# Performance work log

Measured on AMD Instinct MI355X. Metric: run time of the kernel, lower is better.

## Reference

```python
import jax, jax.numpy as jnp
import numpy as np

N_NODES = 100000
N_EDGES = 1600000
NEG_SLOPE = 0.2


def gat_conv(x, W, al, ar, src, dst, n_nodes):
    """DGL-style GATConv. x:[N,Fin] W:[Fin,H*D] al,ar:[H,D] -> [N,H,D]."""
    H, D = al.shape
    h = (x @ W).reshape(-1, H, D)                      # [N,H,D]
    el = jnp.sum(h * al, axis=-1)                      # [N,H]
    er = jnp.sum(h * ar, axis=-1)                      # [N,H]
    e = jax.nn.leaky_relu(el[src] + er[dst], NEG_SLOPE)  # [E,H]
    # segment softmax over edges grouped by destination node
    m = jax.ops.segment_max(e, dst, num_segments=n_nodes)  # [N,H]
    ex = jnp.exp(e - m[dst])                           # [E,H]
    s = jax.ops.segment_sum(ex, dst, num_segments=n_nodes)  # [N,H]
    alpha = ex / s[dst]                                # [E,H]
    msg = h[src] * alpha[..., None]                    # [E,H,D]
    return jax.ops.segment_sum(msg, dst, num_segments=n_nodes)  # [N,H,D]


def setup_inputs() -> dict:
    key = jax.random.key(0)
    ks = jax.random.split(key, 9)
    in_dim, hid, out_dim, heads = 128, 32, 64, 4
    x = jax.random.normal(ks[0], (N_NODES, in_dim), dtype=jnp.float32)
    src = jax.random.randint(ks[1], (N_EDGES,), 0, N_NODES, dtype=jnp.int32)
    dst = jax.random.randint(ks[2], (N_EDGES,), 0, N_NODES, dtype=jnp.int32)
    sc1 = 1.0 / np.sqrt(in_dim)
    sc2 = 1.0 / np.sqrt(heads * hid)
    W1 = jax.random.normal(ks[3], (in_dim, heads * hid), dtype=jnp.float32) * sc1
    al1 = jax.random.normal(ks[4], (heads, hid), dtype=jnp.float32) * sc1
    ar1 = jax.random.normal(ks[5], (heads, hid), dtype=jnp.float32) * sc1
    W2 = jax.random.normal(ks[6], (heads * hid, out_dim), dtype=jnp.float32) * sc2
    al2 = jax.random.normal(ks[7], (1, out_dim), dtype=jnp.float32) * sc2
    ar2 = jax.random.normal(ks[8], (1, out_dim), dtype=jnp.float32) * sc2
    return {"x": x, "src": src, "dst": dst, "W1": W1, "al1": al1, "ar1": ar1,
            "W2": W2, "al2": al2, "ar2": ar2}


def reference(x, src, dst, W1, al1, ar1, W2, al2, ar2):
    h = gat_conv(x, W1, al1, ar1, src, dst, N_NODES)   # [N,4,32]
    h = h.reshape(h.shape[0], -1)                      # flatten(1) -> [N,128]
    h = jax.nn.selu(h)                                 # dropout is identity in eval
    out = gat_conv(h, W2, al2, ar2, src, dst, N_NODES) # [N,1,64]
    return out.mean(axis=1)                            # [N,64]
```

## Files before the change

kernel.cpp:

```cpp
#include <hip/hip_runtime.h>
#include <hip/hip_fp16.h>

#define N_NODES 100000
#define N_EDGES 1600000
#define NP1 (N_NODES + 1)
#define SCANB 512
#define NB 391
#define CHUNK 6250
#define NBLK 256

static __device__ __forceinline__ unsigned pkh2(float a, float b) {
    __half2 t = __floats2half2_rn(a, b);
    return *(unsigned*)&t;
}

__global__ __launch_bounds__(256) void k_gemm1(
    const float* __restrict__ x, const float* __restrict__ W,
    const float* __restrict__ al, const float* __restrict__ ar,
    __half* __restrict__ h, float* __restrict__ el, float* __restrict__ er)
{
    __shared__ float xT[32 * 132];
    __shared__ float Wl[32 * 132];
    const int tid = threadIdx.x;
    const int n0 = blockIdx.x * 128;
    const int tc = tid & 15, tr = tid >> 4;
    const int r0 = tr * 8, c0 = tc * 8;

    float acc[8][8];
    #pragma unroll
    for (int i = 0; i < 8; ++i)
        #pragma unroll
        for (int j = 0; j < 8; ++j) acc[i][j] = 0.f;

    for (int kb = 0; kb < 128; kb += 32) {
        {
            const int k4 = (tid & 7) * 4;
            const int rr = tid >> 3;
            #pragma unroll
            for (int ii = 0; ii < 4; ++ii) {
                int row = rr + ii * 32;
                int n = n0 + row;
                float4 v = make_float4(0.f, 0.f, 0.f, 0.f);
                if (n < N_NODES) v = *(const float4*)(x + (size_t)n * 128 + kb + k4);
                xT[(k4 + 0) * 132 + row] = v.x;
                xT[(k4 + 1) * 132 + row] = v.y;
                xT[(k4 + 2) * 132 + row] = v.z;
                xT[(k4 + 3) * 132 + row] = v.w;
            }
        }
        {
            const int c4 = (tid & 31) * 4;
            const int kr = tid >> 5;
            #pragma unroll
            for (int ii = 0; ii < 4; ++ii) {
                int kk = kr + ii * 8;
                float4 w = *(const float4*)(W + (size_t)(kb + kk) * 128 + c4);
                *(float4*)(Wl + kk * 132 + c4) = w;
            }
        }
        __syncthreads();
        #pragma unroll 4
        for (int k = 0; k < 32; ++k) {
            float4 a0 = *(const float4*)(xT + k * 132 + r0);
            float4 a1 = *(const float4*)(xT + k * 132 + r0 + 4);
            float4 b0 = *(const float4*)(Wl + k * 132 + c0);
            float4 b1 = *(const float4*)(Wl + k * 132 + c0 + 4);
            float a[8] = {a0.x, a0.y, a0.z, a0.w, a1.x, a1.y, a1.z, a1.w};
            float b[8] = {b0.x, b0.y, b0.z, b0.w, b1.x, b1.y, b1.z, b1.w};
            #pragma unroll
            for (int i = 0; i < 8; ++i)
                #pragma unroll
                for (int j = 0; j < 8; ++j) acc[i][j] = fmaf(a[i], b[j], acc[i][j]);
        }
        __syncthreads();
    }

    float alv[8], arv[8];
    #pragma unroll
    for (int j = 0; j < 8; ++j) { alv[j] = al[c0 + j]; arv[j] = ar[c0 + j]; }
    #pragma unroll
    for (int i = 0; i < 8; ++i) {
        int n = n0 + r0 + i;
        float pl = 0.f, pr = 0.f;
        #pragma unroll
        for (int j = 0; j < 8; ++j) {
            pl = fmaf(acc[i][j], alv[j], pl);
            pr = fmaf(acc[i][j], arv[j], pr);
        }
        pl += __shfl_xor(pl, 1); pl += __shfl_xor(pl, 2);
        pr += __shfl_xor(pr, 1); pr += __shfl_xor(pr, 2);
        if (n < N_NODES) {
            uint4 o;
            o.x = pkh2(acc[i][0], acc[i][1]);
            o.y = pkh2(acc[i][2], acc[i][3]);
            o.z = pkh2(acc[i][4], acc[i][5]);
            o.w = pkh2(acc[i][6], acc[i][7]);
            *(uint4*)(h + (size_t)n * 128 + c0) = o;
            if ((tc & 3) == 0) {
                el[n * 4 + (tc >> 2)] = pl;
                er[n * 4 + (tc >> 2)] = pr;
            }
        }
    }
}

__global__ __launch_bounds__(256) void k_gemm2(
    const __half* __restrict__ in, const float* __restrict__ W,
    const float* __restrict__ al, const float* __restrict__ ar,
    __half* __restrict__ h, float* __restrict__ el, float* __restrict__ er)
{
    __shared__ float xT[32 * 132];
    __shared__ float Wl[32 * 68];
    const int tid = threadIdx.x;
    const int n0 = blockIdx.x * 128;
    const int tc = tid & 7, tr = tid >> 3;
    const int r0 = tr * 4, c0 = tc * 8;
    const float SC = 1.0507009873554805f;
    const float AL = 1.6732632423543772f;

    float acc[4][8];
    #pragma unroll
    for (int i = 0; i < 4; ++i)
        #pragma unroll
        for (int j = 0; j < 8; ++j) acc[i][j] = 0.f;

    for (int kb = 0; kb < 128; kb += 32) {
        {
            const int k4 = (tid & 7) * 4;
            const int rr = tid >> 3;
            #pragma unroll
            for (int ii = 0; ii < 4; ++ii) {
                int row = rr + ii * 32;
                int n = n0 + row;
                float4 v = make_float4(0.f, 0.f, 0.f, 0.f);
                if (n < N_NODES) {
                    uint2 u = *(const uint2*)(in + (size_t)n * 128 + kb + k4);
                    float2 f01 = __half22float2(*(__half2*)&u.x);
                    float2 f23 = __half22float2(*(__half2*)&u.y);
                    v = make_float4(f01.x, f01.y, f23.x, f23.y);
                }
                v.x = v.x > 0.f ? SC * v.x : SC * AL * (__expf(v.x) - 1.f);
                v.y = v.y > 0.f ? SC * v.y : SC * AL * (__expf(v.y) - 1.f);
                v.z = v.z > 0.f ? SC * v.z : SC * AL * (__expf(v.z) - 1.f);
                v.w = v.w > 0.f ? SC * v.w : SC * AL * (__expf(v.w) - 1.f);
                xT[(k4 + 0) * 132 + row] = v.x;
                xT[(k4 + 1) * 132 + row] = v.y;
                xT[(k4 + 2) * 132 + row] = v.z;
                xT[(k4 + 3) * 132 + row] = v.w;
            }
        }
        {
            const int c4 = (tid & 15) * 4;
            const int kr = tid >> 4;
            #pragma unroll
            for (int ii = 0; ii < 2; ++ii) {
                int kk = kr + ii * 16;
                float4 w = *(const float4*)(W + (size_t)(kb + kk) * 64 + c4);
                *(float4*)(Wl + kk * 68 + c4) = w;
            }
        }
        __syncthreads();
        #pragma unroll 4
        for (int k = 0; k < 32; ++k) {
            float4 a0 = *(const float4*)(xT + k * 132 + r0);
            float4 b0 = *(const float4*)(Wl + k * 68 + c0);
            float4 b1 = *(const float4*)(Wl + k * 68 + c0 + 4);
            float a[4] = {a0.x, a0.y, a0.z, a0.w};
            float b[8] = {b0.x, b0.y, b0.z, b0.w, b1.x, b1.y, b1.z, b1.w};
            #pragma unroll
            for (int i = 0; i < 4; ++i)
                #pragma unroll
                for (int j = 0; j < 8; ++j) acc[i][j] = fmaf(a[i], b[j], acc[i][j]);
        }
        __syncthreads();
    }

    float alv[8], arv[8];
    #pragma unroll
    for (int j = 0; j < 8; ++j) { alv[j] = al[c0 + j]; arv[j] = ar[c0 + j]; }
    #pragma unroll
    for (int i = 0; i < 4; ++i) {
        int n = n0 + r0 + i;
        float pl = 0.f, pr = 0.f;
        #pragma unroll
        for (int j = 0; j < 8; ++j) {
            pl = fmaf(acc[i][j], alv[j], pl);
            pr = fmaf(acc[i][j], arv[j], pr);
        }
        pl += __shfl_xor(pl, 1); pl += __shfl_xor(pl, 2); pl += __shfl_xor(pl, 4);
        pr += __shfl_xor(pr, 1); pr += __shfl_xor(pr, 2); pr += __shfl_xor(pr, 4);
        if (n < N_NODES) {
            uint4 o;
            o.x = pkh2(acc[i][0], acc[i][1]);
            o.y = pkh2(acc[i][2], acc[i][3]);
            o.z = pkh2(acc[i][4], acc[i][5]);
            o.w = pkh2(acc[i][6], acc[i][7]);
            *(uint4*)(h + (size_t)n * 64 + c0) = o;
            if (tc == 0) { el[n] = pl; er[n] = pr; }
        }
    }
}

__global__ __launch_bounds__(SCANB) void k_scan1(
    int* __restrict__ data, int* __restrict__ bsum, int n)
{
    __shared__ int tmp[SCANB];
    int gid = blockIdx.x * SCANB + threadIdx.x;
    int v = (gid < n) ? data[gid] : 0;
    tmp[threadIdx.x] = v;
    __syncthreads();
    for (int off = 1; off < SCANB; off <<= 1) {
        int t = (threadIdx.x >= off) ? tmp[threadIdx.x - off] : 0;
        __syncthreads();
        tmp[threadIdx.x] += t;
        __syncthreads();
    }
    if (gid < n) data[gid] = tmp[threadIdx.x] - v;
    if (threadIdx.x == SCANB - 1) bsum[blockIdx.x] = tmp[SCANB - 1];
}

__global__ __launch_bounds__(256) void k_scan2(int* __restrict__ bsum, int nb)
{
    __shared__ int tmp[256];
    int v = (threadIdx.x < nb) ? bsum[threadIdx.x] : 0;
    tmp[threadIdx.x] = v;
    __syncthreads();
    for (int off = 1; off < 256; off <<= 1) {
        int t = (threadIdx.x >= off) ? tmp[threadIdx.x - off] : 0;
        __syncthreads();
        tmp[threadIdx.x] += t;
        __syncthreads();
    }
    if (threadIdx.x < nb) bsum[threadIdx.x] = tmp[threadIdx.x] - v;
}

__global__ __launch_bounds__(SCANB) void k_scan3(
    int* __restrict__ data, const int* __restrict__ bsum, int n)
{
    int gid = blockIdx.x * SCANB + threadIdx.x;
    if (gid < n) data[gid] += bsum[blockIdx.x];
}

__global__ __launch_bounds__(256) void k_bhist(
    const int* __restrict__ dst, int* __restrict__ bhist)
{
    __shared__ int cnt[NB];
    const int tid = threadIdx.x;
    for (int j = tid; j < NB; j += 256) cnt[j] = 0;
    __syncthreads();
    int beg = blockIdx.x * CHUNK, end = beg + CHUNK;
    for (int i = beg + tid; i < end; i += 256)
        atomicAdd(&cnt[dst[i] >> 8], 1);
    __syncthreads();
    for (int j = tid; j < NB; j += 256)
        bhist[j * NBLK + blockIdx.x] = cnt[j];
}

__global__ __launch_bounds__(256) void k_place(
    const int* __restrict__ src, const int* __restrict__ dst,
    const int* __restrict__ boffs, unsigned* __restrict__ pairs)
{
    __shared__ int cur[NB];
    const int tid = threadIdx.x;
    for (int j = tid; j < NB; j += 256)
        cur[j] = boffs[j * NBLK + blockIdx.x];
    __syncthreads();
    int beg = blockIdx.x * CHUNK, end = beg + CHUNK;
    for (int i = beg + tid; i < end; i += 256) {
        int d = dst[i];
        int p = atomicAdd(&cur[d >> 8], 1);
        pairs[p] = ((unsigned)(d & 255) << 17) | (unsigned)src[i];
    }
}

__global__ __launch_bounds__(256) void k_csr(
    const unsigned* __restrict__ pairs, const int* __restrict__ boffs,
    int* __restrict__ rowptr, int* __restrict__ csr_src)
{
    __shared__ int cnt[256], exc[256];
    const int b = blockIdx.x;
    const int tid = threadIdx.x;
    cnt[tid] = 0;
    __syncthreads();
    int beg = boffs[b * NBLK];
    int end = (b == NB - 1) ? N_EDGES : boffs[(b + 1) * NBLK];
    for (int i = beg + tid; i < end; i += 256)
        atomicAdd(&cnt[pairs[i] >> 17], 1);
    __syncthreads();
    int v = cnt[tid];
    exc[tid] = v;
    __syncthreads();
    for (int o = 1; o < 256; o <<= 1) {
        int t = (tid >= o) ? exc[tid - o] : 0;
        __syncthreads();
        exc[tid] += t;
        __syncthreads();
    }
    int excl = exc[tid] - v;
    int node = b * 256 + tid;
    if (node <= N_NODES) rowptr[node] = beg + excl;
    __syncthreads();
    exc[tid] = beg + excl;
    cnt[tid] = 0;
    __syncthreads();
    for (int i = beg + tid; i < end; i += 256) {
        unsigned e = pairs[i];
        int dl = (int)(e >> 17);
        int r = atomicAdd(&cnt[dl], 1);
        csr_src[exc[dl] + r] = (int)(e & 0x1FFFFu);
    }
}

__global__ __launch_bounds__(256) void k_fused1(
    const int* __restrict__ rowptr, const int* __restrict__ csr_src,
    const __half* __restrict__ h,
    const float* __restrict__ el,
    const float* __restrict__ er,
    __half* __restrict__ out)
{
    __shared__ int   s_sx[4][64];
    __shared__ float s_p[4][64][4];
    const int w = threadIdx.x >> 6;
    int node = (blockIdx.x * 256 + threadIdx.x) >> 6;
    int lane = threadIdx.x & 63;
    if (node >= N_NODES) return;
    int rs = rowptr[node], re = rowptr[node + 1];
    const int q = lane & 15, g = lane >> 4;
    const int hq = q >> 2;
    float4 erd = ((const float4*)er)[node];
    float m0 = -INFINITY, m1 = -INFINITY, m2 = -INFINITY, m3 = -INFINITY;
    float s0 = 0.f, s1 = 0.f, s2 = 0.f, s3 = 0.f;
    float acc[8];
    #pragma unroll
    for (int k = 0; k < 8; ++k) acc[k] = 0.f;

    for (int base = rs; base < re; base += 64) {
        int nch = min(64, re - base);
        int sidx = 0;
        float e0 = -INFINITY, e1 = -INFINITY, e2 = -INFINITY, e3 = -INFINITY;
        if (lane < nch) {
            sidx = csr_src[base + lane];
            float4 l4 = ((const float4*)el)[sidx];
            e0 = l4.x + erd.x; e0 = e0 >= 0.f ? e0 : 0.2f * e0;
            e1 = l4.y + erd.y; e1 = e1 >= 0.f ? e1 : 0.2f * e1;
            e2 = l4.z + erd.z; e2 = e2 >= 0.f ? e2 : 0.2f * e2;
            e3 = l4.w + erd.w; e3 = e3 >= 0.f ? e3 : 0.2f * e3;
        }
        float c0 = e0, c1 = e1, c2 = e2, c3 = e3;
        #pragma unroll
        for (int o = 32; o > 0; o >>= 1) {
            c0 = fmaxf(c0, __shfl_xor(c0, o));
            c1 = fmaxf(c1, __shfl_xor(c1, o));
            c2 = fmaxf(c2, __shfl_xor(c2, o));
            c3 = fmaxf(c3, __shfl_xor(c3, o));
        }
        float n0 = fmaxf(m0, c0), n1 = fmaxf(m1, c1);
        float n2 = fmaxf(m2, c2), n3 = fmaxf(m3, c3);
        float r0 = __expf(m0 - n0), r1 = __expf(m1 - n1);
        float r2 = __expf(m2 - n2), r3 = __expf(m3 - n3);
        float p0 = __expf(e0 - n0), p1 = __expf(e1 - n1);
        float p2 = __expf(e2 - n2), p3 = __expf(e3 - n3);
        s_sx[w][lane] = sidx;
        float4 pv = make_float4(p0, p1, p2, p3);
        *(float4*)&s_p[w][lane][0] = pv;
        float q0 = p0, q1 = p1, q2 = p2, q3 = p3;
        #pragma unroll
        for (int o = 32; o > 0; o >>= 1) {
            q0 += __shfl_xor(q0, o);
            q1 += __shfl_xor(q1, o);
            q2 += __shfl_xor(q2, o);
            q3 += __shfl_xor(q3, o);
        }
        s0 = s0 * r0 + q0; s1 = s1 * r1 + q1;
        s2 = s2 * r2 + q2; s3 = s3 * r3 + q3;
        float rh = hq == 0 ? r0 : hq == 1 ? r1 : hq == 2 ? r2 : r3;
        #pragma unroll
        for (int k = 0; k < 8; ++k) acc[k] *= rh;
        m0 = n0; m1 = n1; m2 = n2; m3 = n3;

        int nit4 = (nch + 15) >> 4;
        for (int t = 0; t < nit4; ++t) {
            int eb = t * 16 + g;
            int sj0 = s_sx[w][eb];
            int sj1 = s_sx[w][eb + 4];
            int sj2 = s_sx[w][eb + 8];
            int sj3 = s_sx[w][eb + 12];
            float a0 = s_p[w][eb][hq];
            float a1 = s_p[w][eb + 4][hq];
            float a2 = s_p[w][eb + 8][hq];
            float a3 = s_p[w][eb + 12][hq];
            uint4 v0 = *((const uint4*)(h + (size_t)sj0 * 128) + q);
            uint4 v1 = *((const uint4*)(h + (size_t)sj1 * 128) + q);
            uint4 v2 = *((const uint4*)(h + (size_t)sj2 * 128) + q);
            uint4 v3 = *((const uint4*)(h + (size_t)sj3 * 128) + q);
            {
                float2 f0 = __half22float2(*(__half2*)&v0.x);
                float2 f1 = __half22float2(*(__half2*)&v0.y);
                float2 f2 = __half22float2(*(__half2*)&v0.z);
                float2 f3 = __half22float2(*(__half2*)&v0.w);
                acc[0] = fmaf(a0, f0.x, acc[0]); acc[1] = fmaf(a0, f0.y, acc[1]);
                acc[2] = fmaf(a0, f1.x, acc[2]); acc[3] = fmaf(a0, f1.y, acc[3]);
                acc[4] = fmaf(a0, f2.x, acc[4]); acc[5] = fmaf(a0, f2.y, acc[5]);
                acc[6] = fmaf(a0, f3.x, acc[6]); acc[7] = fmaf(a0, f3.y, acc[7]);
            }
            {
                float2 f0 = __half22float2(*(__half2*)&v1.x);
                float2 f1 = __half22float2(*(__half2*)&v1.y);
                float2 f2 = __half22float2(*(__half2*)&v1.z);
                float2 f3 = __half22float2(*(__half2*)&v1.w);
                acc[0] = fmaf(a1, f0.x, acc[0]); acc[1] = fmaf(a1, f0.y, acc[1]);
                acc[2] = fmaf(a1, f1.x, acc[2]); acc[3] = fmaf(a1, f1.y, acc[3]);
                acc[4] = fmaf(a1, f2.x, acc[4]); acc[5] = fmaf(a1, f2.y, acc[5]);
                acc[6] = fmaf(a1, f3.x, acc[6]); acc[7] = fmaf(a1, f3.y, acc[7]);
            }
            {
                float2 f0 = __half22float2(*(__half2*)&v2.x);
                float2 f1 = __half22float2(*(__half2*)&v2.y);
                float2 f2 = __half22float2(*(__half2*)&v2.z);
                float2 f3 = __half22float2(*(__half2*)&v2.w);
                acc[0] = fmaf(a2, f0.x, acc[0]); acc[1] = fmaf(a2, f0.y, acc[1]);
                acc[2] = fmaf(a2, f1.x, acc[2]); acc[3] = fmaf(a2, f1.y, acc[3]);
                acc[4] = fmaf(a2, f2.x, acc[4]); acc[5] = fmaf(a2, f2.y, acc[5]);
                acc[6] = fmaf(a2, f3.x, acc[6]); acc[7] = fmaf(a2, f3.y, acc[7]);
            }
            {
                float2 f0 = __half22float2(*(__half2*)&v3.x);
                float2 f1 = __half22float2(*(__half2*)&v3.y);
                float2 f2 = __half22float2(*(__half2*)&v3.z);
                float2 f3 = __half22float2(*(__half2*)&v3.w);
                acc[0] = fmaf(a3, f0.x, acc[0]); acc[1] = fmaf(a3, f0.y, acc[1]);
                acc[2] = fmaf(a3, f1.x, acc[2]); acc[3] = fmaf(a3, f1.y, acc[3]);
                acc[4] = fmaf(a3, f2.x, acc[4]); acc[5] = fmaf(a3, f2.y, acc[5]);
                acc[6] = fmaf(a3, f3.x, acc[6]); acc[7] = fmaf(a3, f3.y, acc[7]);
            }
        }
    }
    float sh = hq == 0 ? s0 : hq == 1 ? s1 : hq == 2 ? s2 : s3;
    float inv = (re > rs) ? 1.f / sh : 0.f;
    #pragma unroll
    for (int k = 0; k < 8; ++k) {
        acc[k] *= inv;
        acc[k] += __shfl_xor(acc[k], 16);
        acc[k] += __shfl_xor(acc[k], 32);
    }
    if (g == 0) {
        uint4 o;
        o.x = pkh2(acc[0], acc[1]);
        o.y = pkh2(acc[2], acc[3]);
        o.z = pkh2(acc[4], acc[5]);
        o.w = pkh2(acc[6], acc[7]);
        *((uint4*)(out + (size_t)node * 128) + q) = o;
    }
}

__global__ __launch_bounds__(256) void k_fused2(
    const int* __restrict__ rowptr, const int* __restrict__ csr_src,
    const __half* __restrict__ h,
    const float* __restrict__ el,
    const float* __restrict__ er,
    float* __restrict__ out)
{
    __shared__ int   s_sx[4][64];
    __shared__ float s_p[4][64];
    const int w = threadIdx.x >> 6;
    int node = (blockIdx.x * 256 + threadIdx.x) >> 6;
    int lane = threadIdx.x & 63;
    if (node >= N_NODES) return;
    int rs = rowptr[node], re = rowptr[node + 1];
    const int q = lane & 7, g = lane >> 3;
    float erd = er[node];
    float m = -INFINITY, s = 0.f;
    float acc[8];
    #pragma unroll
    for (int k = 0; k < 8; ++k) acc[k] = 0.f;

    for (int base = rs; base < re; base += 64) {
        int nch = min(64, re - base);
        int sidx = 0;
        float e = -INFINITY;
        if (lane < nch) {
            sidx = csr_src[base + lane];
            e = el[sidx] + erd;
            e = e >= 0.f ? e : 0.2f * e;
        }
        float c = e;
        #pragma unroll
        for (int o = 32; o > 0; o >>= 1) c = fmaxf(c, __shfl_xor(c, o));
        float n = fmaxf(m, c);
        float r = __expf(m - n);
        float p = __expf(e - n);
        s_sx[w][lane] = sidx;
        s_p[w][lane] = p;
        float qq = p;
        #pragma unroll
        for (int o = 32; o > 0; o >>= 1) qq += __shfl_xor(qq, o);
        s = s * r + qq;
        #pragma unroll
        for (int k = 0; k < 8; ++k) acc[k] *= r;
        m = n;

        int nit4 = (nch + 31) >> 5;
        for (int t = 0; t < nit4; ++t) {
            int eb = t * 32 + g;
            int sj0 = s_sx[w][eb];
            int sj1 = s_sx[w][eb + 8];
            int sj2 = s_sx[w][eb + 16];
            int sj3 = s_sx[w][eb + 24];
            float a0 = s_p[w][eb];
            float a1 = s_p[w][eb + 8];
            float a2 = s_p[w][eb + 16];
            float a3 = s_p[w][eb + 24];
            uint4 v0 = *((const uint4*)(h + (size_t)sj0 * 64) + q);
            uint4 v1 = *((const uint4*)(h + (size_t)sj1 * 64) + q);
            uint4 v2 = *((const uint4*)(h + (size_t)sj2 * 64) + q);
            uint4 v3 = *((const uint4*)(h + (size_t)sj3 * 64) + q);
            {
                float2 f0 = __half22float2(*(__half2*)&v0.x);
                float2 f1 = __half22float2(*(__half2*)&v0.y);
                float2 f2 = __half22float2(*(__half2*)&v0.z);
                float2 f3 = __half22float2(*(__half2*)&v0.w);
                acc[0] = fmaf(a0, f0.x, acc[0]); acc[1] = fmaf(a0, f0.y, acc[1]);
                acc[2] = fmaf(a0, f1.x, acc[2]); acc[3] = fmaf(a0, f1.y, acc[3]);
                acc[4] = fmaf(a0, f2.x, acc[4]); acc[5] = fmaf(a0, f2.y, acc[5]);
                acc[6] = fmaf(a0, f3.x, acc[6]); acc[7] = fmaf(a0, f3.y, acc[7]);
            }
            {
                float2 f0 = __half22float2(*(__half2*)&v1.x);
                float2 f1 = __half22float2(*(__half2*)&v1.y);
                float2 f2 = __half22float2(*(__half2*)&v1.z);
                float2 f3 = __half22float2(*(__half2*)&v1.w);
                acc[0] = fmaf(a1, f0.x, acc[0]); acc[1] = fmaf(a1, f0.y, acc[1]);
                acc[2] = fmaf(a1, f1.x, acc[2]); acc[3] = fmaf(a1, f1.y, acc[3]);
                acc[4] = fmaf(a1, f2.x, acc[4]); acc[5] = fmaf(a1, f2.y, acc[5]);
                acc[6] = fmaf(a1, f3.x, acc[6]); acc[7] = fmaf(a1, f3.y, acc[7]);
            }
            {
                float2 f0 = __half22float2(*(__half2*)&v2.x);
                float2 f1 = __half22float2(*(__half2*)&v2.y);
                float2 f2 = __half22float2(*(__half2*)&v2.z);
                float2 f3 = __half22float2(*(__half2*)&v2.w);
                acc[0] = fmaf(a2, f0.x, acc[0]); acc[1] = fmaf(a2, f0.y, acc[1]);
                acc[2] = fmaf(a2, f1.x, acc[2]); acc[3] = fmaf(a2, f1.y, acc[3]);
                acc[4] = fmaf(a2, f2.x, acc[4]); acc[5] = fmaf(a2, f2.y, acc[5]);
                acc[6] = fmaf(a2, f3.x, acc[6]); acc[7] = fmaf(a2, f3.y, acc[7]);
            }
            {
                float2 f0 = __half22float2(*(__half2*)&v3.x);
                float2 f1 = __half22float2(*(__half2*)&v3.y);
                float2 f2 = __half22float2(*(__half2*)&v3.z);
                float2 f3 = __half22float2(*(__half2*)&v3.w);
                acc[0] = fmaf(a3, f0.x, acc[0]); acc[1] = fmaf(a3, f0.y, acc[1]);
                acc[2] = fmaf(a3, f1.x, acc[2]); acc[3] = fmaf(a3, f1.y, acc[3]);
                acc[4] = fmaf(a3, f2.x, acc[4]); acc[5] = fmaf(a3, f2.y, acc[5]);
                acc[6] = fmaf(a3, f3.x, acc[6]); acc[7] = fmaf(a3, f3.y, acc[7]);
            }
        }
    }
    float inv = (re > rs) ? 1.f / s : 0.f;
    #pragma unroll
    for (int k = 0; k < 8; ++k) {
        acc[k] *= inv;
        acc[k] += __shfl_xor(acc[k], 8);
        acc[k] += __shfl_xor(acc[k], 16);
        acc[k] += __shfl_xor(acc[k], 32);
    }
    if (g == 0) {
        float* op = out + (size_t)node * 64 + q * 8;
        *(float4*)(op)     = make_float4(acc[0], acc[1], acc[2], acc[3]);
        *(float4*)(op + 4) = make_float4(acc[4], acc[5], acc[6], acc[7]);
    }
}

extern "C" void kernel_launch(void* const* d_in, const int* in_sizes, int n_in,
                              void* d_out, int out_size, void* d_ws, size_t ws_size,
                              hipStream_t stream) {
    const float* x   = (const float*)d_in[0];
    const int*   src = (const int*)d_in[1];
    const int*   dst = (const int*)d_in[2];
    const float* W1  = (const float*)d_in[3];
    const float* al1 = (const float*)d_in[4];
    const float* ar1 = (const float*)d_in[5];
    const float* W2  = (const float*)d_in[6];
    const float* al2 = (const float*)d_in[7];
    const float* ar2 = (const float*)d_in[8];
    float* out = (float*)d_out;

    char* base = (char*)d_ws;
    __half* h1   = (__half*)base;   base += (size_t)N_NODES * 128 * 2;
    __half* out1 = (__half*)base;   base += (size_t)N_NODES * 128 * 2;
    float*  el1  = (float*)base;    base += (size_t)N_NODES * 4 * 4;
    float*  er1  = (float*)base;    base += (size_t)N_NODES * 4 * 4;
    int* rowptr  = (int*)base;      base += (size_t)100004 * 4;
    int* bhist   = (int*)base;      base += (size_t)NB * NBLK * 4;
    int* bsum2   = (int*)base;      base += 1024;
    int* csr_src = (int*)base;      base += (size_t)N_EDGES * 4;
    unsigned* pairs = (unsigned*)base; base += (size_t)N_EDGES * 4;
    __half* h2   = h1;
    float*  el2  = (float*)((char*)h1 + (size_t)N_NODES * 64 * 2);
    float*  er2  = el2 + N_NODES;

    const int n2  = NB * NBLK;
    const int nb2 = (n2 + SCANB - 1) / SCANB;
    const int GB  = (N_NODES + 127) / 128;

    k_bhist<<<NBLK, 256, 0, stream>>>(dst, bhist);
    k_scan1<<<nb2, SCANB, 0, stream>>>(bhist, bsum2, n2);
    k_scan2<<<1, 256, 0, stream>>>(bsum2, nb2);
    k_scan3<<<nb2, SCANB, 0, stream>>>(bhist, bsum2, n2);
    k_place<<<NBLK, 256, 0, stream>>>(src, dst, bhist, pairs);
    k_csr<<<NB, 256, 0, stream>>>(pairs, bhist, rowptr, csr_src);

    k_gemm1<<<GB, 256, 0, stream>>>(x, W1, al1, ar1, h1, el1, er1);
    k_fused1<<<(N_NODES + 3) / 4, 256, 0, stream>>>(rowptr, csr_src, h1, el1, er1, out1);

    k_gemm2<<<GB, 256, 0, stream>>>(out1, W2, al2, ar2, h2, el2, er2);
    k_fused2<<<(N_NODES + 3) / 4, 256, 0, stream>>>(rowptr, csr_src, h2, el2, er2, out);
}
```

Measured before the change: 273.1 us.

## Simplify CSR bucketing with atomic cursors, peel first softmax chunk, use fma_mix

Replaces the per-block bucket histogram plus three-kernel scan with a global bucket total, a single-block scan, and per-block atomic cursor reservation in the placement kernel. This cuts kernel launches and scan work during CSR construction. Bucket order within a segment becomes nondeterministic, but k_csr regroups by node so results stay correct up to summation order. The aggregation kernels peel the first 64-edge chunk to skip the online-softmax rescale for low-degree nodes, and use inline v_fma_mix_f32 so fp16 features feed the FMA without separate conversions.

```diff
diff --git a/kernel.cpp b/kernel.cpp
--- a/kernel.cpp
+++ b/kernel.cpp
@@ -4,7 +4,6 @@
 #define N_NODES 100000
 #define N_EDGES 1600000
 #define NP1 (N_NODES + 1)
-#define SCANB 512
 #define NB 391
 #define CHUNK 6250
 #define NBLK 256
@@ -12,6 +11,21 @@
 static __device__ __forceinline__ unsigned pkh2(float a, float b) {
     __half2 t = __floats2half2_rn(a, b);
     return *(unsigned*)&t;
+}
+
+static __device__ __forceinline__ void fmix2(float& a_lo, float& a_hi,
+                                             unsigned hw, float a) {
+    asm("v_fma_mix_f32 %0, %1, %2, %0 op_sel:[0,0,0] op_sel_hi:[1,0,0]"
+        : "+v"(a_lo) : "v"(hw), "v"(a));
+    asm("v_fma_mix_f32 %0, %1, %2, %0 op_sel:[1,0,0] op_sel_hi:[1,0,0]"
+        : "+v"(a_hi) : "v"(hw), "v"(a));
+}
+
+static __device__ __forceinline__ void fmix8(float* acc, uint4 v, float a) {
+    fmix2(acc[0], acc[1], v.x, a);
+    fmix2(acc[2], acc[3], v.y, a);
+    fmix2(acc[4], acc[5], v.z, a);
+    fmix2(acc[6], acc[7], v.w, a);
 }
 
 __global__ __launch_bounds__(256) void k_gemm1(
@@ -201,48 +215,8 @@
     }
 }
 
-__global__ __launch_bounds__(SCANB) void k_scan1(
-    int* __restrict__ data, int* __restrict__ bsum, int n)
-{
-    __shared__ int tmp[SCANB];
-    int gid = blockIdx.x * SCANB + threadIdx.x;
-    int v = (gid < n) ? data[gid] : 0;
-    tmp[threadIdx.x] = v;
-    __syncthreads();
-    for (int off = 1; off < SCANB; off <<= 1) {
-        int t = (threadIdx.x >= off) ? tmp[threadIdx.x - off] : 0;
-        __syncthreads();
-        tmp[threadIdx.x] += t;
-        __syncthreads();
-    }
-    if (gid < n) data[gid] = tmp[threadIdx.x] - v;
-    if (threadIdx.x == SCANB - 1) bsum[blockIdx.x] = tmp[SCANB - 1];
-}
-
-__global__ __launch_bounds__(256) void k_scan2(int* __restrict__ bsum, int nb)
-{
-    __shared__ int tmp[256];
-    int v = (threadIdx.x < nb) ? bsum[threadIdx.x] : 0;
-    tmp[threadIdx.x] = v;
-    __syncthreads();
-    for (int off = 1; off < 256; off <<= 1) {
-        int t = (threadIdx.x >= off) ? tmp[threadIdx.x - off] : 0;
-        __syncthreads();
-        tmp[threadIdx.x] += t;
-        __syncthreads();
-    }
-    if (threadIdx.x < nb) bsum[threadIdx.x] = tmp[threadIdx.x] - v;
-}
-
-__global__ __launch_bounds__(SCANB) void k_scan3(
-    int* __restrict__ data, const int* __restrict__ bsum, int n)
-{
-    int gid = blockIdx.x * SCANB + threadIdx.x;
-    if (gid < n) data[gid] += bsum[blockIdx.x];
-}
-
-__global__ __launch_bounds__(256) void k_bhist(
-    const int* __restrict__ dst, int* __restrict__ bhist)
+__global__ __launch_bounds__(256) void k_bhist_tot(
+    const int* __restrict__ dst, int* __restrict__ btot)
 {
     __shared__ int cnt[NB];
     const int tid = threadIdx.x;
@@ -253,23 +227,49 @@
         atomicAdd(&cnt[dst[i] >> 8], 1);
     __syncthreads();
     for (int j = tid; j < NB; j += 256)
-        bhist[j * NBLK + blockIdx.x] = cnt[j];
+        if (cnt[j]) atomicAdd(&btot[j], cnt[j]);
+}
+
+__global__ __launch_bounds__(512) void k_bscan(
+    const int* __restrict__ btot, int* __restrict__ boffs, int* __restrict__ cursor)
+{
+    __shared__ int tmp[512];
+    int t = threadIdx.x;
+    int v = (t < NB) ? btot[t] : 0;
+    tmp[t] = v;
+    __syncthreads();
+    for (int o = 1; o < 512; o <<= 1) {
+        int u = (t >= o) ? tmp[t - o] : 0;
+        __syncthreads();
+        tmp[t] += u;
+        __syncthreads();
+    }
+    if (t < NB) { boffs[t] = tmp[t] - v; cursor[t] = tmp[t] - v; }
+    if (t == 0) boffs[NB] = N_EDGES;
 }
 
 __global__ __launch_bounds__(256) void k_place(
     const int* __restrict__ src, const int* __restrict__ dst,
-    const int* __restrict__ boffs, unsigned* __restrict__ pairs)
-{
-    __shared__ int cur[NB];
+    int* __restrict__ cursor, unsigned* __restrict__ pairs)
+{
+    __shared__ int cnt[NB], basev[NB];
     const int tid = threadIdx.x;
+    for (int j = tid; j < NB; j += 256) cnt[j] = 0;
+    __syncthreads();
+    int beg = blockIdx.x * CHUNK, end = beg + CHUNK;
+    for (int i = beg + tid; i < end; i += 256)
+        atomicAdd(&cnt[dst[i] >> 8], 1);
+    __syncthreads();
     for (int j = tid; j < NB; j += 256)
-        cur[j] = boffs[j * NBLK + blockIdx.x];
-    __syncthreads();
-    int beg = blockIdx.x * CHUNK, end = beg + CHUNK;
+        basev[j] = cnt[j] ? atomicAdd(&cursor[j], cnt[j]) : 0;
+    __syncthreads();
+    for (int j = tid; j < NB; j += 256) cnt[j] = 0;
+    __syncthreads();
     for (int i = beg + tid; i < end; i += 256) {
         int d = dst[i];
-        int p = atomicAdd(&cur[d >> 8], 1);
-        pairs[p] = ((unsigned)(d & 255) << 17) | (unsigned)src[i];
+        int b = d >> 8;
+        int r = atomicAdd(&cnt[b], 1);
+        pairs[basev[b] + r] = ((unsigned)(d & 255) << 17) | (unsigned)src[i];
     }
 }
 
@@ -282,8 +282,8 @@
     const int tid = threadIdx.x;
     cnt[tid] = 0;
     __syncthreads();
-    int beg = boffs[b * NBLK];
-    int end = (b == NB - 1) ? N_EDGES : boffs[(b + 1) * NBLK];
+    int beg = boffs[b];
+    int end = boffs[b + 1];
     for (int i = beg + tid; i < end; i += 256)
         atomicAdd(&cnt[pairs[i] >> 17], 1);
     __syncthreads();
@@ -321,63 +321,20 @@
     __shared__ int   s_sx[4][64];
     __shared__ float s_p[4][64][4];
     const int w = threadIdx.x >> 6;
-    int node = (blockIdx.x * 256 + threadIdx.x) >> 6;
+    int node = (blockIdx.x << 2) + w;
     int lane = threadIdx.x & 63;
     if (node >= N_NODES) return;
     int rs = rowptr[node], re = rowptr[node + 1];
     const int q = lane & 15, g = lane >> 4;
     const int hq = q >> 2;
     float4 erd = ((const float4*)er)[node];
-    float m0 = -INFINITY, m1 = -INFINITY, m2 = -INFINITY, m3 = -INFINITY;
+    float m0, m1, m2, m3;
     float s0 = 0.f, s1 = 0.f, s2 = 0.f, s3 = 0.f;
     float acc[8];
     #pragma unroll
     for (int k = 0; k < 8; ++k) acc[k] = 0.f;
 
-    for (int base = rs; base < re; base += 64) {
-        int nch = min(64, re - base);
-        int sidx = 0;
-        float e0 = -INFINITY, e1 = -INFINITY, e2 = -INFINITY, e3 = -INFINITY;
-        if (lane < nch) {
-            sidx = csr_src[base + lane];
-            float4 l4 = ((const float4*)el)[sidx];
-            e0 = l4.x + erd.x; e0 = e0 >= 0.f ? e0 : 0.2f * e0;
-            e1 = l4.y + erd.y; e1 = e1 >= 0.f ? e1 : 0.2f * e1;
-            e2 = l4.z + erd.z; e2 = e2 >= 0.f ? e2 : 0.2f * e2;
-            e3 = l4.w + erd.w; e3 = e3 >= 0.f ? e3 : 0.2f * e3;
-        }
-        float c0 = e0, c1 = e1, c2 = e2, c3 = e3;
-        #pragma unroll
-        for (int o = 32; o > 0; o >>= 1) {
-            c0 = fmaxf(c0, __shfl_xor(c0, o));
-            c1 = fmaxf(c1, __shfl_xor(c1, o));
-            c2 = fmaxf(c2, __shfl_xor(c2, o));
-            c3 = fmaxf(c3, __shfl_xor(c3, o));
-        }
-        float n0 = fmaxf(m0, c0), n1 = fmaxf(m1, c1);
-        float n2 = fmaxf(m2, c2), n3 = fmaxf(m3, c3);
-        float r0 = __expf(m0 - n0), r1 = __expf(m1 - n1);
-        float r2 = __expf(m2 - n2), r3 = __expf(m3 - n3);
-        float p0 = __expf(e0 - n0), p1 = __expf(e1 - n1);
-        float p2 = __expf(e2 - n2), p3 = __expf(e3 - n3);
-        s_sx[w][lane] = sidx;
-        float4 pv = make_float4(p0, p1, p2, p3);
-        *(float4*)&s_p[w][lane][0] = pv;
-        float q0 = p0, q1 = p1, q2 = p2, q3 = p3;
-        #pragma unroll
-        for (int o = 32; o > 0; o >>= 1) {
-            q0 += __shfl_xor(q0, o);
-            q1 += __shfl_xor(q1, o);
-            q2 += __shfl_xor(q2, o);
-            q3 += __shfl_xor(q3, o);
-        }
-        s0 = s0 * r0 + q0; s1 = s1 * r1 + q1;
-        s2 = s2 * r2 + q2; s3 = s3 * r3 + q3;
-        float rh = hq == 0 ? r0 : hq == 1 ? r1 : hq == 2 ? r2 : r3;
-        #pragma unroll
-        for (int k = 0; k < 8; ++k) acc[k] *= rh;
-        m0 = n0; m1 = n1; m2 = n2; m3 = n3;
-
+    auto agg = [&](int nch) {
         int nit4 = (nch + 15) >> 4;
         for (int t = 0; t < nit4; ++t) {
             int eb = t * 16 + g;
@@ -393,48 +350,95 @@
             uint4 v1 = *((const uint4*)(h + (size_t)sj1 * 128) + q);
             uint4 v2 = *((const uint4*)(h + (size_t)sj2 * 128) + q);
             uint4 v3 = *((const uint4*)(h + (size_t)sj3 * 128) + q);
-            {
-                float2 f0 = __half22float2(*(__half2*)&v0.x);
-                float2 f1 = __half22float2(*(__half2*)&v0.y);
-                float2 f2 = __half22float2(*(__half2*)&v0.z);
-                float2 f3 = __half22float2(*(__half2*)&v0.w);
-                acc[0] = fmaf(a0, f0.x, acc[0]); acc[1] = fmaf(a0, f0.y, acc[1]);
-                acc[2] = fmaf(a0, f1.x, acc[2]); acc[3] = fmaf(a0, f1.y, acc[3]);
-                acc[4] = fmaf(a0, f2.x, acc[4]); acc[5] = fmaf(a0, f2.y, acc[5]);
-                acc[6] = fmaf(a0, f3.x, acc[6]); acc[7] = fmaf(a0, f3.y, acc[7]);
-            }
-            {
-                float2 f0 = __half22float2(*(__half2*)&v1.x);
-                float2 f1 = __half22float2(*(__half2*)&v1.y);
-                float2 f2 = __half22float2(*(__half2*)&v1.z);
-                float2 f3 = __half22float2(*(__half2*)&v1.w);
-                acc[0] = fmaf(a1, f0.x, acc[0]); acc[1] = fmaf(a1, f0.y, acc[1]);
-                acc[2] = fmaf(a1, f1.x, acc[2]); acc[3] = fmaf(a1, f1.y, acc[3]);
-                acc[4] = fmaf(a1, f2.x, acc[4]); acc[5] = fmaf(a1, f2.y, acc[5]);
-                acc[6] = fmaf(a1, f3.x, acc[6]); acc[7] = fmaf(a1, f3.y, acc[7]);
-            }
-            {
-                float2 f0 = __half22float2(*(__half2*)&v2.x);
-                float2 f1 = __half22float2(*(__half2*)&v2.y);
-                float2 f2 = __half22float2(*(__half2*)&v2.z);
-                float2 f3 = __half22float2(*(__half2*)&v2.w);
-                acc[0] = fmaf(a2, f0.x, acc[0]); acc[1] = fmaf(a2, f0.y, acc[1]);
-                acc[2] = fmaf(a2, f1.x, acc[2]); acc[3] = fmaf(a2, f1.y, acc[3]);
-                acc[4] = fmaf(a2, f2.x, acc[4]); acc[5] = fmaf(a2, f2.y, acc[5]);
-                acc[6] = fmaf(a2, f3.x, acc[6]); acc[7] = fmaf(a2, f3.y, acc[7]);
-            }
-            {
-                float2 f0 = __half22float2(*(__half2*)&v3.x);
-                float2 f1 = __half22float2(*(__half2*)&v3.y);
-                float2 f2 = __half22float2(*(__half2*)&v3.z);
-                float2 f3 = __half22float2(*(__half2*)&v3.w);
-                acc[0] = fmaf(a3, f0.x, acc[0]); acc[1] = fmaf(a3, f0.y, acc[1]);
-                acc[2] = fmaf(a3, f1.x, acc[2]); acc[3] = fmaf(a3, f1.y, acc[3]);
-                acc[4] = fmaf(a3, f2.x, acc[4]); acc[5] = fmaf(a3, f2.y, acc[5]);
-                acc[6] = fmaf(a3, f3.x, acc[6]); acc[7] = fmaf(a3, f3.y, acc[7]);
-            }
-        }
-    }
+            fmix8(acc, v0, a0);
+            fmix8(acc, v1, a1);
+            fmix8(acc, v2, a2);
+            fmix8(acc, v3, a3);
+        }
+    };
+
+    if (re > rs) {
+        int nch = min(64, re - rs);
+        int sidx = 0;
+        float e0 = -INFINITY, e1 = -INFINITY, e2 = -INFINITY, e3 = -INFINITY;
+        if (lane < nch) {
+            sidx = csr_src[rs + lane];
+            float4 l4 = ((const float4*)el)[sidx];
+            e0 = l4.x + erd.x; e0 = e0 >= 0.f ? e0 : 0.2f * e0;
+            e1 = l4.y + erd.y; e1 = e1 >= 0.f ? e1 : 0.2f * e1;
+            e2 = l4.z + erd.z; e2 = e2 >= 0.f ? e2 : 0.2f * e2;
+            e3 = l4.w + erd.w; e3 = e3 >= 0.f ? e3 : 0.2f * e3;
+        }
+        float c0 = e0, c1 = e1, c2 = e2, c3 = e3;
+        #pragma unroll
+        for (int o = 32; o > 0; o >>= 1) {
+            c0 = fmaxf(c0, __shfl_xor(c0, o));
+            c1 = fmaxf(c1, __shfl_xor(c1, o));
+            c2 = fmaxf(c2, __shfl_xor(c2, o));
+            c3 = fmaxf(c3, __shfl_xor(c3, o));
+        }
+        m0 = c0; m1 = c1; m2 = c2; m3 = c3;
+        float p0 = __expf(e0 - m0), p1 = __expf(e1 - m1);
+        float p2 = __expf(e2 - m2), p3 = __expf(e3 - m3);
+        s_sx[w][lane] = sidx;
+        *(float4*)&s_p[w][lane][0] = make_float4(p0, p1, p2, p3);
+        float q0 = p0, q1 = p1, q2 = p2, q3 = p3;
+        #pragma unroll
+        for (int o = 32; o > 0; o >>= 1) {
+            q0 += __shfl_xor(q0, o);
+            q1 += __shfl_xor(q1, o);
+            q2 += __shfl_xor(q2, o);
+            q3 += __shfl_xor(q3, o);
+        }
+        s0 = q0; s1 = q1; s2 = q2; s3 = q3;
+        agg(nch);
+
+        for (int base = rs + 64; base < re; base += 64) {
+            nch = min(64, re - base);
+            sidx = 0;
+            e0 = e1 = e2 = e3 = -INFINITY;
+            if (lane < nch) {
+                sidx = csr_src[base + lane];
+                float4 l4 = ((const float4*)el)[sidx];
+                e0 = l4.x + erd.x; e0 = e0 >= 0.f ? e0 : 0.2f * e0;
+                e1 = l4.y + erd.y; e1 = e1 >= 0.f ? e1 : 0.2f * e1;
+                e2 = l4.z + erd.z; e2 = e2 >= 0.f ? e2 : 0.2f * e2;
+                e3 = l4.w + erd.w; e3 = e3 >= 0.f ? e3 : 0.2f * e3;
+            }
+            c0 = e0; c1 = e1; c2 = e2; c3 = e3;
+            #pragma unroll
+            for (int o = 32; o > 0; o >>= 1) {
+                c0 = fmaxf(c0, __shfl_xor(c0, o));
+                c1 = fmaxf(c1, __shfl_xor(c1, o));
+                c2 = fmaxf(c2, __shfl_xor(c2, o));
+                c3 = fmaxf(c3, __shfl_xor(c3, o));
+            }
+            float n0 = fmaxf(m0, c0), n1 = fmaxf(m1, c1);
+            float n2 = fmaxf(m2, c2), n3 = fmaxf(m3, c3);
+            float r0 = __expf(m0 - n0), r1 = __expf(m1 - n1);
+            float r2 = __expf(m2 - n2), r3 = __expf(m3 - n3);
+            p0 = __expf(e0 - n0); p1 = __expf(e1 - n1);
+            p2 = __expf(e2 - n2); p3 = __expf(e3 - n3);
+            s_sx[w][lane] = sidx;
+            *(float4*)&s_p[w][lane][0] = make_float4(p0, p1, p2, p3);
+            q0 = p0; q1 = p1; q2 = p2; q3 = p3;
+            #pragma unroll
+            for (int o = 32; o > 0; o >>= 1) {
+                q0 += __shfl_xor(q0, o);
+                q1 += __shfl_xor(q1, o);
+                q2 += __shfl_xor(q2, o);
+                q3 += __shfl_xor(q3, o);
+            }
+            s0 = s0 * r0 + q0; s1 = s1 * r1 + q1;
+            s2 = s2 * r2 + q2; s3 = s3 * r3 + q3;
+            float rh = hq == 0 ? r0 : hq == 1 ? r1 : hq == 2 ? r2 : r3;
+            #pragma unroll
+            for (int k = 0; k < 8; ++k) acc[k] *= rh;
+            m0 = n0; m1 = n1; m2 = n2; m3 = n3;
+            agg(nch);
+        }
+    }
+
     float sh = hq == 0 ? s0 : hq == 1 ? s1 : hq == 2 ? s2 : s3;
     float inv = (re > rs) ? 1.f / sh : 0.f;
     #pragma unroll
@@ -463,42 +467,18 @@
     __shared__ int   s_sx[4][64];
     __shared__ float s_p[4][64];
     const int w = threadIdx.x >> 6;
-    int node = (blockIdx.x * 256 + threadIdx.x) >> 6;
+    int node = (blockIdx.x << 2) + w;
     int lane = threadIdx.x & 63;
     if (node >= N_NODES) return;
     int rs = rowptr[node], re = rowptr[node + 1];
     const int q = lane & 7, g = lane >> 3;
     float erd = er[node];
-    float m = -INFINITY, s = 0.f;
+    float m, s = 0.f;
     float acc[8];
     #pragma unroll
     for (int k = 0; k < 8; ++k) acc[k] = 0.f;
 
-    for (int base = rs; base < re; base += 64) {
-        int nch = min(64, re - base);
-        int sidx = 0;
-        float e = -INFINITY;
-        if (lane < nch) {
-            sidx = csr_src[base + lane];
-            e = el[sidx] + erd;
-            e = e >= 0.f ? e : 0.2f * e;
-        }
-        float c = e;
-        #pragma unroll
-        for (int o = 32; o > 0; o >>= 1) c = fmaxf(c, __shfl_xor(c, o));
-        float n = fmaxf(m, c);
-        float r = __expf(m - n);
-        float p = __expf(e - n);
-        s_sx[w][lane] = sidx;
-        s_p[w][lane] = p;
-        float qq = p;
-        #pragma unroll
-        for (int o = 32; o > 0; o >>= 1) qq += __shfl_xor(qq, o);
-        s = s * r + qq;
-        #pragma unroll
-        for (int k = 0; k < 8; ++k) acc[k] *= r;
-        m = n;
-
+    auto agg = [&](int nch) {
         int nit4 = (nch + 31) >> 5;
         for (int t = 0; t < nit4; ++t) {
             int eb = t * 32 + g;
@@ -514,48 +494,63 @@
             uint4 v1 = *((const uint4*)(h + (size_t)sj1 * 64) + q);
             uint4 v2 = *((const uint4*)(h + (size_t)sj2 * 64) + q);
             uint4 v3 = *((const uint4*)(h + (size_t)sj3 * 64) + q);
-            {
-                float2 f0 = __half22float2(*(__half2*)&v0.x);
-                float2 f1 = __half22float2(*(__half2*)&v0.y);
-                float2 f2 = __half22float2(*(__half2*)&v0.z);
-                float2 f3 = __half22float2(*(__half2*)&v0.w);
-                acc[0] = fmaf(a0, f0.x, acc[0]); acc[1] = fmaf(a0, f0.y, acc[1]);
-                acc[2] = fmaf(a0, f1.x, acc[2]); acc[3] = fmaf(a0, f1.y, acc[3]);
-                acc[4] = fmaf(a0, f2.x, acc[4]); acc[5] = fmaf(a0, f2.y, acc[5]);
-                acc[6] = fmaf(a0, f3.x, acc[6]); acc[7] = fmaf(a0, f3.y, acc[7]);
-            }
-            {
-                float2 f0 = __half22float2(*(__half2*)&v1.x);
-                float2 f1 = __half22float2(*(__half2*)&v1.y);
-                float2 f2 = __half22float2(*(__half2*)&v1.z);
-                float2 f3 = __half22float2(*(__half2*)&v1.w);
-                acc[0] = fmaf(a1, f0.x, acc[0]); acc[1] = fmaf(a1, f0.y, acc[1]);
-                acc[2] = fmaf(a1, f1.x, acc[2]); acc[3] = fmaf(a1, f1.y, acc[3]);
-                acc[4] = fmaf(a1, f2.x, acc[4]); acc[5] = fmaf(a1, f2.y, acc[5]);
-                acc[6] = fmaf(a1, f3.x, acc[6]); acc[7] = fmaf(a1, f3.y, acc[7]);
-            }
-            {
-                float2 f0 = __half22float2(*(__half2*)&v2.x);
-                float2 f1 = __half22float2(*(__half2*)&v2.y);
-                float2 f2 = __half22float2(*(__half2*)&v2.z);
-                float2 f3 = __half22float2(*(__half2*)&v2.w);
-                acc[0] = fmaf(a2, f0.x, acc[0]); acc[1] = fmaf(a2, f0.y, acc[1]);
-                acc[2] = fmaf(a2, f1.x, acc[2]); acc[3] = fmaf(a2, f1.y, acc[3]);
-                acc[4] = fmaf(a2, f2.x, acc[4]); acc[5] = fmaf(a2, f2.y, acc[5]);
-                acc[6] = fmaf(a2, f3.x, acc[6]); acc[7] = fmaf(a2, f3.y, acc[7]);
-            }
-            {
-                float2 f0 = __half22float2(*(__half2*)&v3.x);
-                float2 f1 = __half22float2(*(__half2*)&v3.y);
-                float2 f2 = __half22float2(*(__half2*)&v3.z);
-                float2 f3 = __half22float2(*(__half2*)&v3.w);
-                acc[0] = fmaf(a3, f0.x, acc[0]); acc[1] = fmaf(a3, f0.y, acc[1]);
-                acc[2] = fmaf(a3, f1.x, acc[2]); acc[3] = fmaf(a3, f1.y, acc[3]);
-                acc[4] = fmaf(a3, f2.x, acc[4]); acc[5] = fmaf(a3, f2.y, acc[5]);
-                acc[6] = fmaf(a3, f3.x, acc[6]); acc[7] = fmaf(a3, f3.y, acc[7]);
-            }
-        }
-    }
+            fmix8(acc, v0, a0);
+            fmix8(acc, v1, a1);
+            fmix8(acc, v2, a2);
+            fmix8(acc, v3, a3);
+        }
+    };
+
+    if (re > rs) {
+        int nch = min(64, re - rs);
+        int sidx = 0;
+        float e = -INFINITY;
+        if (lane < nch) {
+            sidx = csr_src[rs + lane];
+            e = el[sidx] + erd;
+            e = e >= 0.f ? e : 0.2f * e;
+        }
+        float c = e;
+        #pragma unroll
+        for (int o = 32; o > 0; o >>= 1) c = fmaxf(c, __shfl_xor(c, o));
+        m = c;
+        float p = __expf(e - m);
+        s_sx[w][lane] = sidx;
+        s_p[w][lane] = p;
+        float qq = p;
+        #pragma unroll
+        for (int o = 32; o > 0; o >>= 1) qq += __shfl_xor(qq, o);
+        s = qq;
+        agg(nch);
+
+        for (int base = rs + 64; base < re; base += 64) {
+            nch = min(64, re - base);
+            sidx = 0;
+            e = -INFINITY;
+            if (lane < nch) {
+                sidx = csr_src[base + lane];
+                e = el[sidx] + erd;
+                e = e >= 0.f ? e : 0.2f * e;
+            }
+            c = e;
+            #pragma unroll
+            for (int o = 32; o > 0; o >>= 1) c = fmaxf(c, __shfl_xor(c, o));
+            float n = fmaxf(m, c);
+            float r = __expf(m - n);
+            p = __expf(e - n);
+            s_sx[w][lane] = sidx;
+            s_p[w][lane] = p;
+            float qq2 = p;
+            #pragma unroll
+            for (int o = 32; o > 0; o >>= 1) qq2 += __shfl_xor(qq2, o);
+            s = s * r + qq2;
+            #pragma unroll
+            for (int k = 0; k < 8; ++k) acc[k] *= r;
+            m = n;
+            agg(nch);
+        }
+    }
+
     float inv = (re > rs) ? 1.f / s : 0.f;
     #pragma unroll
     for (int k = 0; k < 8; ++k) {
@@ -591,24 +586,22 @@
     float*  el1  = (float*)base;    base += (size_t)N_NODES * 4 * 4;
     float*  er1  = (float*)base;    base += (size_t)N_NODES * 4 * 4;
     int* rowptr  = (int*)base;      base += (size_t)100004 * 4;
-    int* bhist   = (int*)base;      base += (size_t)NB * NBLK * 4;
-    int* bsum2   = (int*)base;      base += 1024;
+    int* btot    = (int*)base;      base += 512 * 4;
+    int* boffs   = (int*)base;      base += 512 * 4;
+    int* cursor  = (int*)base;      base += 512 * 4;
     int* csr_src = (int*)base;      base += (size_t)N_EDGES * 4;
     unsigned* pairs = (unsigned*)base; base += (size_t)N_EDGES * 4;
     __half* h2   = h1;
     float*  el2  = (float*)((char*)h1 + (size_t)N_NODES * 64 * 2);
     float*  er2  = el2 + N_NODES;
 
-    const int n2  = NB * NBLK;
-    const int nb2 = (n2 + SCANB - 1) / SCANB;
-    const int GB  = (N_NODES + 127) / 128;
-
-    k_bhist<<<NBLK, 256, 0, stream>>>(dst, bhist);
-    k_scan1<<<nb2, SCANB, 0, stream>>>(bhist, bsum2, n2);
-    k_scan2<<<1, 256, 0, stream>>>(bsum2, nb2);
-    k_scan3<<<nb2, SCANB, 0, stream>>>(bhist, bsum2, n2);
-    k_place<<<NBLK, 256, 0, stream>>>(src, dst, bhist, pairs);
-    k_csr<<<NB, 256, 0, stream>>>(pairs, bhist, rowptr, csr_src);
+    const int GB = (N_NODES + 127) / 128;
+
+    hipMemsetAsync(btot, 0, NB * sizeof(int), stream);
+    k_bhist_tot<<<NBLK, 256, 0, stream>>>(dst, btot);
+    k_bscan<<<1, 512, 0, stream>>>(btot, boffs, cursor);
+    k_place<<<NBLK, 256, 0, stream>>>(src, dst, cursor, pairs);
+    k_csr<<<NB, 256, 0, stream>>>(pairs, boffs, rowptr, csr_src);
 
     k_gemm1<<<GB, 256, 0, stream>>>(x, W1, al1, ar1, h1, el1, er1);
     k_fused1<<<(N_NODES + 3) / 4, 256, 0, stream>>>(rowptr, csr_src, h1, el1, er1, out1);
```

Result: no change. 272.6 us (-0.2%).
